# Kernel tuning notes

Hardware: AMD Instinct MI355X
Metric: run time of the kernel (lower is better)

## Reference

```python
import jax, jax.numpy as jnp
import numpy as np

N, D, T = 4096, 256, 8
RHO = 16.0
DT = 1.0 / T


def setup_inputs() -> dict:
    key = jax.random.key(0)
    k1, k2, k3, k4 = jax.random.split(key, 4)
    X = jax.random.normal(k1, (N, D), dtype=jnp.float32)
    # learned deformation parameters (small init so the Euler flow stays stable)
    A = jax.random.normal(k2, (T, N, D), dtype=jnp.float32) * 0.01
    A_aff = jax.random.normal(k3, (T, D, D), dtype=jnp.float32) * 0.01
    b_aff = jax.random.normal(k4, (T, D), dtype=jnp.float32) * 0.01
    return {"X": X, "A": A, "A_aff": A_aff, "b_aff": b_aff}


def _flow(X, A, A_aff, b_aff):
    inv_two_rho2 = 1.0 / (2.0 * RHO * RHO)

    def step(Z, params_t):
        A_t, Aaff_t, baff_t = params_t
        # Gaussian self-kernel K[i,j] = exp(-||z_i - z_j||^2 / (2 rho^2))
        sq = jnp.sum(Z * Z, axis=1)                      # [n]
        dist = sq[:, None] + sq[None, :] - 2.0 * (Z @ Z.T)  # [n, n]
        K = jnp.exp(-dist * inv_two_rho2)
        # velocity: affine part + RKHS (kernel message aggregation) part
        v = Z @ Aaff_t.T + baff_t[None, :] + K @ A_t     # [n, d]
        return Z + DT * v, None

    Z_final, _ = jax.lax.scan(step, X, (A, A_aff, b_aff))
    return Z_final


def reference(X, A, A_aff, b_aff):
    return _flow(X, A, A_aff, b_aff)
```

## Files before the change

kernel.cpp:

```cpp
#include <hip/hip_runtime.h>


#define N_PTS 4096
#define DIM   256
#define DT_C  0.125f
#define C1    (1.0f/512.0f)

typedef __bf16 bf16x8 __attribute__((ext_vector_type(8)));
typedef float  f32x16 __attribute__((ext_vector_type(16)));
typedef float  f32x4v __attribute__((ext_vector_type(4)));
typedef unsigned int   u32x4 __attribute__((ext_vector_type(4)));
typedef unsigned short u16x8 __attribute__((ext_vector_type(8)));

__device__ __forceinline__ unsigned short f2bf(float f) {
  unsigned int u = __builtin_bit_cast(unsigned int, f);
  u += 0x7fffu + ((u >> 16) & 1u);
  return (unsigned short)(u >> 16);
}
__device__ __forceinline__ float bf2f(unsigned short s) {
  unsigned int u = ((unsigned int)s) << 16;
  return __builtin_bit_cast(float, u);
}

__global__ __launch_bounds__(256) void k_prep(const float* __restrict__ A,
                                              unsigned short* __restrict__ ATf) {
  __shared__ float sT[64][36];
  const int jgrp = blockIdx.x, ds = blockIdx.y, t = blockIdx.z;
  const int tid = threadIdx.x;
  const float* Ab = A + (size_t)t * N_PTS * DIM;
  {
    const int j_l = tid >> 2, dq = tid & 3;
    const float* src = Ab + (size_t)(jgrp * 64 + j_l) * DIM + ds * 32 + dq * 8;
    f32x4v v0 = *(const f32x4v*)src, v1 = *(const f32x4v*)(src + 4);
    *(f32x4v*)&sT[j_l][dq * 8] = v0;
    *(f32x4v*)&sT[j_l][dq * 8 + 4] = v1;
  }
  __syncthreads();
  const int jb_l = tid >> 6, l = tid & 63, l31 = l & 31, lhi = l >> 5;
  u16x8 o;
#pragma unroll
  for (int e = 0; e < 8; ++e) o[e] = f2bf(sT[jb_l * 16 + lhi * 8 + e][l31]);
  unsigned short* dst = ATf + (size_t)t * (8 * 256 * 64 * 8)
                      + ((size_t)(ds * 256 + jgrp * 4 + jb_l) * 64 + l) * 8;
  *(u16x8*)dst = o;
}

__global__ __launch_bounds__(256) void k_init(const float* __restrict__ X,
                                              unsigned short* __restrict__ Zf,
                                              float* __restrict__ erow) {
  const int tid = threadIdx.x;
  const int r = blockIdx.x * 8 + (tid >> 5), o = tid & 31;
  const size_t base = (size_t)r * DIM + o * 8;
  f32x4v z0 = *(const f32x4v*)(X + base), z1 = *(const f32x4v*)(X + base + 4);
  u16x8 zb; float s = 0.f;
#pragma unroll
  for (int i = 0; i < 4; ++i) { zb[i] = f2bf(z0[i]); zb[4 + i] = f2bf(z1[i]);
                                s += z0[i] * z0[i] + z1[i] * z1[i]; }
  *(u16x8*)(Zf + ((size_t)((r >> 5) * 16 + (o >> 1)) * 64 + (o & 1) * 32 + (r & 31)) * 8) = zb;
#pragma unroll
  for (int d = 16; d > 0; d >>= 1) s += __shfl_down(s, d, 32);
  if (o == 0) erow[r] = __expf(-s * C1);
}

__global__ __launch_bounds__(512, 2) void k_flash(
    const unsigned short* __restrict__ Zf, const float* __restrict__ erow,
    const unsigned short* __restrict__ ATf_t,
    const float* __restrict__ Aaff_t,
    unsigned short* __restrict__ Opart) {
  __shared__ unsigned short sAj[3][32 * 512];
  __shared__ unsigned short sP[2][128 * 64];

  const int tid = threadIdx.x, lane = tid & 63, wid = tid >> 6;
  const int l31 = lane & 31, lhi = lane >> 5;
  const int chunk = blockIdx.x;
  const int i0 = blockIdx.y * 128;
  const int jb16 = chunk * 32;

#define STAGE(nt)                                                              \
  {                                                                            \
    unsigned short* dstb = sAj[(nt) % 3];                                      \
    _Pragma("unroll")                                                          \
    for (int q = 0; q < 4; ++q) {                                              \
      int s = wid * 4 + q;                                                     \
      int ds_ = s >> 2, ksl = s & 3;                                           \
      const unsigned short* src = ATf_t +                                      \
          ((size_t)(ds_ * 256 + jb16 + (nt) * 4 + ksl) * 64 + lane) * 8;       \
      *(u32x4*)&dstb[s * 512 + lane * 8] = *(const u32x4*)src;                 \
    }                                                                          \
  }

  STAGE(0);
  __syncthreads();

  if (wid < 4) {
    const int g1 = wid;
    bf16x8 af[16];
    {
      const unsigned short* ap = Zf + (((size_t)((i0 >> 5) + g1) * 16) * 64 + lane) * 8;
#pragma unroll
      for (int ks = 0; ks < 16; ++ks)
        af[ks] = __builtin_bit_cast(bf16x8, *(const u32x4*)(ap + ks * 512));
    }
    float eI[16];
#pragma unroll
    for (int c = 0; c < 16; ++c)
      eI[c] = erow[i0 + g1 * 32 + 4 * lhi + (c & 3) + 8 * (c >> 2)];

    for (int n = 0; n <= 8; ++n) {
      if (n < 8) {
        if (n < 7) STAGE(n + 1);
        f32x16 S0, S1;
#pragma unroll
        for (int i = 0; i < 16; ++i) { S0[i] = 0.f; S1[i] = 0.f; }
        {
          const unsigned short* bp =
              Zf + (((size_t)(chunk * 16 + n * 2) * 16) * 64 + lane) * 8;
#pragma unroll
          for (int ks = 0; ks < 16; ++ks) {
            bf16x8 b0 = __builtin_bit_cast(bf16x8, *(const u32x4*)(bp + ks * 512));
            bf16x8 b1 = __builtin_bit_cast(bf16x8, *(const u32x4*)(bp + 8192 + ks * 512));
            S0 = __builtin_amdgcn_mfma_f32_32x32x16_bf16(af[ks], b0, S0, 0, 0, 0);
            S1 = __builtin_amdgcn_mfma_f32_32x32x16_bf16(af[ks], b1, S1, 0, 0, 0);
          }
        }
        const int jj0 = chunk * 512 + n * 64;
        const float ej0 = erow[jj0 + l31];
        const float ej1 = erow[jj0 + 32 + l31];
        unsigned short* pb = sP[n & 1];
        const int blk0 = l31 >> 3, cl = l31 & 7;
#pragma unroll
        for (int c = 0; c < 16; ++c) {
          const int row = g1 * 32 + 4 * lhi + (c & 3) + 8 * (c >> 2);
          pb[row * 64 + ((blk0 ^ (row & 7)) * 8) + cl] =
              f2bf(eI[c] * ej0 * __expf(2.f * C1 * S0[c]));
          pb[row * 64 + (((4 + blk0) ^ (row & 7)) * 8) + cl] =
              f2bf(eI[c] * ej1 * __expf(2.f * C1 * S1[c]));
        }
      }
      __syncthreads();
    }
  } else {
    const int w4 = wid - 4;
    f32x16 Oa[4][2];
#pragma unroll
    for (int rs = 0; rs < 4; ++rs)
#pragma unroll
      for (int ct = 0; ct < 2; ++ct)
#pragma unroll
        for (int i = 0; i < 16; ++i) Oa[rs][ct][i] = 0.f;

    for (int n = 0; n <= 8; ++n) {
      if (n < 7) STAGE(n + 1);
      if (n == 0) {
#pragma unroll
        for (int q = 0; q < 2; ++q) {
          const int ksg = chunk * 2 + q;
          bf16x8 a[4];
#pragma unroll
          for (int rs = 0; rs < 4; ++rs)
            a[rs] = __builtin_bit_cast(bf16x8, *(const u32x4*)(
                Zf + (((size_t)((i0 >> 5) + rs) * 16 + ksg) * 64 + lane) * 8));
#pragma unroll
          for (int ct = 0; ct < 2; ++ct) {
            const int d = w4 * 64 + ct * 32 + l31;
            const float* bp = Aaff_t + (size_t)d * DIM + ksg * 16 + lhi * 8;
            f32x4v f0 = *(const f32x4v*)bp, f1 = *(const f32x4v*)(bp + 4);
            u16x8 tb;
#pragma unroll
            for (int i = 0; i < 4; ++i) { tb[i] = f2bf(f0[i]); tb[4 + i] = f2bf(f1[i]); }
            bf16x8 bv = __builtin_bit_cast(bf16x8, tb);
#pragma unroll
            for (int rs = 0; rs < 4; ++rs)
              Oa[rs][ct] = __builtin_amdgcn_mfma_f32_32x32x16_bf16(a[rs], bv, Oa[rs][ct], 0, 0, 0);
          }
        }
      }
      if (n >= 1) {
        const int m = n - 1;
        const unsigned short* aj = sAj[m % 3];
        const unsigned short* pb = sP[m & 1];
#pragma unroll
        for (int ks = 0; ks < 4; ++ks) {
          bf16x8 a[4], b[2];
          const int blk = ks * 2 + lhi;
#pragma unroll
          for (int rs = 0; rs < 4; ++rs) {
            const int row = rs * 32 + l31;
            a[rs] = *(const bf16x8*)&pb[row * 64 + ((blk ^ (row & 7)) * 8)];
          }
#pragma unroll
          for (int ct = 0; ct < 2; ++ct)
            b[ct] = *(const bf16x8*)&aj[((w4 * 2 + ct) * 4 + ks) * 512 + lane * 8];
#pragma unroll
          for (int rs = 0; rs < 4; ++rs)
#pragma unroll
            for (int ct = 0; ct < 2; ++ct)
              Oa[rs][ct] = __builtin_amdgcn_mfma_f32_32x32x16_bf16(a[rs], b[ct], Oa[rs][ct], 0, 0, 0);
        }
      }
      __syncthreads();
    }
    unsigned short* ob = Opart + (size_t)chunk * N_PTS * DIM + (size_t)w4 * 64 + l31;
#pragma unroll
    for (int rs = 0; rs < 4; ++rs)
#pragma unroll
      for (int cg = 0; cg < 4; ++cg) {
        const int rbase = rs * 32 + 4 * lhi + 8 * cg;
#pragma unroll
        for (int e = 0; e < 4; ++e) {
          const int c = cg * 4 + e;
          const size_t ro = (size_t)(i0 + rbase + e) * DIM;
          ob[ro]      = f2bf(Oa[rs][0][c]);
          ob[ro + 32] = f2bf(Oa[rs][1][c]);
        }
      }
  }
#undef STAGE
}

__global__ __launch_bounds__(256) void k_update(const float* __restrict__ Zin,
                                                const unsigned short* __restrict__ Opart,
                                                const float* __restrict__ baff_t,
                                                float* __restrict__ Zout,
                                                unsigned short* __restrict__ Zf,
                                                float* __restrict__ erow) {
  const int tid = threadIdx.x;
  const int r = blockIdx.x * 8 + (tid >> 5), o = tid & 31;
  const size_t base = (size_t)r * DIM + o * 8;
  f32x4v z0 = *(const f32x4v*)(Zin + base), z1 = *(const f32x4v*)(Zin + base + 4);
  f32x4v s0 = *(const f32x4v*)(baff_t + o * 8), s1 = *(const f32x4v*)(baff_t + o * 8 + 4);
#pragma unroll
  for (int c = 0; c < 8; ++c) {
    u16x8 p = *(const u16x8*)(Opart + (size_t)c * N_PTS * DIM + base);
#pragma unroll
    for (int i = 0; i < 4; ++i) { s0[i] += bf2f(p[i]); s1[i] += bf2f(p[4 + i]); }
  }
  u16x8 zb; float sv = 0.f;
#pragma unroll
  for (int i = 0; i < 4; ++i) {
    z0[i] += DT_C * s0[i]; z1[i] += DT_C * s1[i];
    zb[i] = f2bf(z0[i]); zb[4 + i] = f2bf(z1[i]);
    sv += z0[i] * z0[i] + z1[i] * z1[i];
  }
  *(f32x4v*)(Zout + base) = z0;
  *(f32x4v*)(Zout + base + 4) = z1;
  *(u16x8*)(Zf + ((size_t)((r >> 5) * 16 + (o >> 1)) * 64 + (o & 1) * 32 + (r & 31)) * 8) = zb;
#pragma unroll
  for (int d = 16; d > 0; d >>= 1) sv += __shfl_down(sv, d, 32);
  if (o == 0) erow[r] = __expf(-sv * C1);
}

extern "C" void kernel_launch(void* const* d_in, const int* in_sizes, int n_in,
                              void* d_out, int out_size, void* d_ws, size_t ws_size,
                              hipStream_t stream) {
  const float* X    = (const float*)d_in[0];
  const float* A    = (const float*)d_in[1];
  const float* Aaff = (const float*)d_in[2];
  const float* baff = (const float*)d_in[3];
  float* out = (float*)d_out;

  char* w = (char*)d_ws;
  size_t off = 0;
  unsigned short* ATf = (unsigned short*)(w + off); off += (size_t)8 * 8 * 256 * 64 * 8 * 2;
  unsigned short* Zf  = (unsigned short*)(w + off); off += (size_t)N_PTS * DIM * 2;
  float* erow = (float*)(w + off); off += (size_t)N_PTS * 4;
  float* Zf32 = (float*)(w + off); off += (size_t)N_PTS * DIM * 4;
  unsigned short* Opart = (unsigned short*)(w + off); off += (size_t)8 * N_PTS * DIM * 2;
  (void)ws_size; (void)in_sizes; (void)n_in; (void)out_size;

  k_prep<<<dim3(64, 8, 8), 256, 0, stream>>>(A, ATf);
  k_init<<<512, 256, 0, stream>>>(X, Zf, erow);

  const float* zin = X;
  for (int t = 0; t < 8; ++t) {
    float* zout = (t == 7) ? out : Zf32;
    k_flash<<<dim3(8, 32), 512, 0, stream>>>(
        Zf, erow, ATf + (size_t)t * (8 * 256 * 64 * 8), Aaff + (size_t)t * DIM * DIM, Opart);
    k_update<<<512, 256, 0, stream>>>(zin, Opart, baff + (size_t)t * DIM, zout, Zf, erow);
    zin = zout;
  }
}
```

Measured before the change: 430.3 us.

## Halve row tile per block, drop LDS staging of A, double grid

The flash kernel now handles 64 query rows per block instead of 128, and the launch grid doubles to 8x64 blocks. Each S-producing wave now computes one 32x32 tile instead of two. The triple-buffered shared-memory staging of the A operand is removed; consumer waves read A fragments directly from global memory. Launch bounds are raised to 4 blocks per CU. This is meant to improve occupancy and parallelism, but A is now re-read from global or L2 twice as often, and each block does less work per sync.

```diff
diff --git a/kernel.cpp b/kernel.cpp
--- a/kernel.cpp
+++ b/kernel.cpp
@@ -62,41 +62,24 @@
   if (o == 0) erow[r] = __expf(-s * C1);
 }
 
-__global__ __launch_bounds__(512, 2) void k_flash(
+__global__ __launch_bounds__(512, 4) void k_flash(
     const unsigned short* __restrict__ Zf, const float* __restrict__ erow,
     const unsigned short* __restrict__ ATf_t,
     const float* __restrict__ Aaff_t,
     unsigned short* __restrict__ Opart) {
-  __shared__ unsigned short sAj[3][32 * 512];
-  __shared__ unsigned short sP[2][128 * 64];
+  __shared__ unsigned short sP[2][64 * 64];
 
   const int tid = threadIdx.x, lane = tid & 63, wid = tid >> 6;
   const int l31 = lane & 31, lhi = lane >> 5;
   const int chunk = blockIdx.x;
-  const int i0 = blockIdx.y * 128;
-  const int jb16 = chunk * 32;
-
-#define STAGE(nt)                                                              \
-  {                                                                            \
-    unsigned short* dstb = sAj[(nt) % 3];                                      \
-    _Pragma("unroll")                                                          \
-    for (int q = 0; q < 4; ++q) {                                              \
-      int s = wid * 4 + q;                                                     \
-      int ds_ = s >> 2, ksl = s & 3;                                           \
-      const unsigned short* src = ATf_t +                                      \
-          ((size_t)(ds_ * 256 + jb16 + (nt) * 4 + ksl) * 64 + lane) * 8;       \
-      *(u32x4*)&dstb[s * 512 + lane * 8] = *(const u32x4*)src;                 \
-    }                                                                          \
-  }
-
-  STAGE(0);
-  __syncthreads();
+  const int i0 = blockIdx.y * 64;
+  const int ib = i0 >> 5;
 
   if (wid < 4) {
-    const int g1 = wid;
+    const int ip = wid >> 1, jh = wid & 1;
     bf16x8 af[16];
     {
-      const unsigned short* ap = Zf + (((size_t)((i0 >> 5) + g1) * 16) * 64 + lane) * 8;
+      const unsigned short* ap = Zf + ((size_t)(ib + ip) * 16 * 64 + lane) * 8;
 #pragma unroll
       for (int ks = 0; ks < 16; ++ks)
         af[ks] = __builtin_bit_cast(bf16x8, *(const u32x4*)(ap + ks * 512));
@@ -104,118 +87,102 @@
     float eI[16];
 #pragma unroll
     for (int c = 0; c < 16; ++c)
-      eI[c] = erow[i0 + g1 * 32 + 4 * lhi + (c & 3) + 8 * (c >> 2)];
-
-    for (int n = 0; n <= 8; ++n) {
-      if (n < 8) {
-        if (n < 7) STAGE(n + 1);
-        f32x16 S0, S1;
-#pragma unroll
-        for (int i = 0; i < 16; ++i) { S0[i] = 0.f; S1[i] = 0.f; }
-        {
-          const unsigned short* bp =
-              Zf + (((size_t)(chunk * 16 + n * 2) * 16) * 64 + lane) * 8;
-#pragma unroll
-          for (int ks = 0; ks < 16; ++ks) {
-            bf16x8 b0 = __builtin_bit_cast(bf16x8, *(const u32x4*)(bp + ks * 512));
-            bf16x8 b1 = __builtin_bit_cast(bf16x8, *(const u32x4*)(bp + 8192 + ks * 512));
-            S0 = __builtin_amdgcn_mfma_f32_32x32x16_bf16(af[ks], b0, S0, 0, 0, 0);
-            S1 = __builtin_amdgcn_mfma_f32_32x32x16_bf16(af[ks], b1, S1, 0, 0, 0);
-          }
+      eI[c] = erow[i0 + ip * 32 + 4 * lhi + (c & 3) + 8 * (c >> 2)];
+
+    for (int n = 0; n < 8; ++n) {
+      f32x16 S;
+#pragma unroll
+      for (int i = 0; i < 16; ++i) S[i] = 0.f;
+      {
+        const int jblk = chunk * 16 + n * 2 + jh;
+        const unsigned short* bp = Zf + ((size_t)jblk * 16 * 64 + lane) * 8;
+#pragma unroll
+        for (int ks = 0; ks < 16; ++ks) {
+          bf16x8 b = __builtin_bit_cast(bf16x8, *(const u32x4*)(bp + ks * 512));
+          S = __builtin_amdgcn_mfma_f32_32x32x16_bf16(af[ks], b, S, 0, 0, 0);
         }
-        const int jj0 = chunk * 512 + n * 64;
-        const float ej0 = erow[jj0 + l31];
-        const float ej1 = erow[jj0 + 32 + l31];
-        unsigned short* pb = sP[n & 1];
-        const int blk0 = l31 >> 3, cl = l31 & 7;
-#pragma unroll
-        for (int c = 0; c < 16; ++c) {
-          const int row = g1 * 32 + 4 * lhi + (c & 3) + 8 * (c >> 2);
-          pb[row * 64 + ((blk0 ^ (row & 7)) * 8) + cl] =
-              f2bf(eI[c] * ej0 * __expf(2.f * C1 * S0[c]));
-          pb[row * 64 + (((4 + blk0) ^ (row & 7)) * 8) + cl] =
-              f2bf(eI[c] * ej1 * __expf(2.f * C1 * S1[c]));
+      }
+      const float ej = erow[chunk * 512 + n * 64 + jh * 32 + l31];
+      unsigned short* pb = sP[n & 1];
+      const int blk = jh * 4 + (l31 >> 3), cl = l31 & 7;
+#pragma unroll
+      for (int c = 0; c < 16; ++c) {
+        const int row = ip * 32 + 4 * lhi + (c & 3) + 8 * (c >> 2);
+        pb[row * 64 + ((blk ^ (row & 7)) * 8) + cl] =
+            f2bf(eI[c] * ej * __expf(2.f * C1 * S[c]));
+      }
+      __syncthreads();
+    }
+    __syncthreads();
+  } else {
+    const int cd = wid - 4;
+    f32x16 O[2][2];
+#pragma unroll
+    for (int rs = 0; rs < 2; ++rs)
+#pragma unroll
+      for (int ct = 0; ct < 2; ++ct)
+#pragma unroll
+        for (int i = 0; i < 16; ++i) O[rs][ct][i] = 0.f;
+
+#pragma unroll
+    for (int q = 0; q < 2; ++q) {
+      const int ksg = chunk * 2 + q;
+      bf16x8 a[2];
+#pragma unroll
+      for (int rs = 0; rs < 2; ++rs)
+        a[rs] = __builtin_bit_cast(bf16x8, *(const u32x4*)(
+            Zf + (((size_t)(ib + rs) * 16 + ksg) * 64 + lane) * 8));
+#pragma unroll
+      for (int ct = 0; ct < 2; ++ct) {
+        const int d = cd * 64 + ct * 32 + l31;
+        const float* bp = Aaff_t + (size_t)d * DIM + ksg * 16 + lhi * 8;
+        f32x4v f0 = *(const f32x4v*)bp, f1 = *(const f32x4v*)(bp + 4);
+        u16x8 tb;
+#pragma unroll
+        for (int i = 0; i < 4; ++i) { tb[i] = f2bf(f0[i]); tb[4 + i] = f2bf(f1[i]); }
+        bf16x8 bv = __builtin_bit_cast(bf16x8, tb);
+#pragma unroll
+        for (int rs = 0; rs < 2; ++rs)
+          O[rs][ct] = __builtin_amdgcn_mfma_f32_32x32x16_bf16(a[rs], bv, O[rs][ct], 0, 0, 0);
+      }
+    }
+    __syncthreads();
+
+    for (int n = 1; n <= 8; ++n) {
+      const int m = n - 1;
+      const unsigned short* pb = sP[m & 1];
+#pragma unroll
+      for (int ks = 0; ks < 4; ++ks) {
+        bf16x8 a[2], b[2];
+        const int blk = ks * 2 + lhi;
+#pragma unroll
+        for (int rs = 0; rs < 2; ++rs) {
+          const int row = rs * 32 + l31;
+          a[rs] = *(const bf16x8*)&pb[row * 64 + ((blk ^ (row & 7)) * 8)];
         }
+#pragma unroll
+        for (int ct = 0; ct < 2; ++ct)
+          b[ct] = __builtin_bit_cast(bf16x8, *(const u32x4*)(ATf_t +
+              ((size_t)((cd * 2 + ct) * 256 + chunk * 32 + m * 4 + ks) * 64 + lane) * 8));
+#pragma unroll
+        for (int rs = 0; rs < 2; ++rs)
+#pragma unroll
+          for (int ct = 0; ct < 2; ++ct)
+            O[rs][ct] = __builtin_amdgcn_mfma_f32_32x32x16_bf16(a[rs], b[ct], O[rs][ct], 0, 0, 0);
       }
       __syncthreads();
     }
-  } else {
-    const int w4 = wid - 4;
-    f32x16 Oa[4][2];
-#pragma unroll
-    for (int rs = 0; rs < 4; ++rs)
-#pragma unroll
-      for (int ct = 0; ct < 2; ++ct)
-#pragma unroll
-        for (int i = 0; i < 16; ++i) Oa[rs][ct][i] = 0.f;
-
-    for (int n = 0; n <= 8; ++n) {
-      if (n < 7) STAGE(n + 1);
-      if (n == 0) {
-#pragma unroll
-        for (int q = 0; q < 2; ++q) {
-          const int ksg = chunk * 2 + q;
-          bf16x8 a[4];
-#pragma unroll
-          for (int rs = 0; rs < 4; ++rs)
-            a[rs] = __builtin_bit_cast(bf16x8, *(const u32x4*)(
-                Zf + (((size_t)((i0 >> 5) + rs) * 16 + ksg) * 64 + lane) * 8));
-#pragma unroll
-          for (int ct = 0; ct < 2; ++ct) {
-            const int d = w4 * 64 + ct * 32 + l31;
-            const float* bp = Aaff_t + (size_t)d * DIM + ksg * 16 + lhi * 8;
-            f32x4v f0 = *(const f32x4v*)bp, f1 = *(const f32x4v*)(bp + 4);
-            u16x8 tb;
-#pragma unroll
-            for (int i = 0; i < 4; ++i) { tb[i] = f2bf(f0[i]); tb[4 + i] = f2bf(f1[i]); }
-            bf16x8 bv = __builtin_bit_cast(bf16x8, tb);
-#pragma unroll
-            for (int rs = 0; rs < 4; ++rs)
-              Oa[rs][ct] = __builtin_amdgcn_mfma_f32_32x32x16_bf16(a[rs], bv, Oa[rs][ct], 0, 0, 0);
-          }
-        }
-      }
-      if (n >= 1) {
-        const int m = n - 1;
-        const unsigned short* aj = sAj[m % 3];
-        const unsigned short* pb = sP[m & 1];
-#pragma unroll
-        for (int ks = 0; ks < 4; ++ks) {
-          bf16x8 a[4], b[2];
-          const int blk = ks * 2 + lhi;
-#pragma unroll
-          for (int rs = 0; rs < 4; ++rs) {
-            const int row = rs * 32 + l31;
-            a[rs] = *(const bf16x8*)&pb[row * 64 + ((blk ^ (row & 7)) * 8)];
-          }
-#pragma unroll
-          for (int ct = 0; ct < 2; ++ct)
-            b[ct] = *(const bf16x8*)&aj[((w4 * 2 + ct) * 4 + ks) * 512 + lane * 8];
-#pragma unroll
-          for (int rs = 0; rs < 4; ++rs)
-#pragma unroll
-            for (int ct = 0; ct < 2; ++ct)
-              Oa[rs][ct] = __builtin_amdgcn_mfma_f32_32x32x16_bf16(a[rs], b[ct], Oa[rs][ct], 0, 0, 0);
-        }
-      }
-      __syncthreads();
-    }
-    unsigned short* ob = Opart + (size_t)chunk * N_PTS * DIM + (size_t)w4 * 64 + l31;
-#pragma unroll
-    for (int rs = 0; rs < 4; ++rs)
-#pragma unroll
-      for (int cg = 0; cg < 4; ++cg) {
-        const int rbase = rs * 32 + 4 * lhi + 8 * cg;
-#pragma unroll
-        for (int e = 0; e < 4; ++e) {
-          const int c = cg * 4 + e;
-          const size_t ro = (size_t)(i0 + rbase + e) * DIM;
-          ob[ro]      = f2bf(Oa[rs][0][c]);
-          ob[ro + 32] = f2bf(Oa[rs][1][c]);
-        }
-      }
-  }
-#undef STAGE
+
+    unsigned short* ob = Opart + (size_t)chunk * N_PTS * DIM + (size_t)cd * 64 + l31;
+#pragma unroll
+    for (int rs = 0; rs < 2; ++rs)
+#pragma unroll
+      for (int c = 0; c < 16; ++c) {
+        const int row = i0 + rs * 32 + 4 * lhi + (c & 3) + 8 * (c >> 2);
+        ob[(size_t)row * DIM]      = f2bf(O[rs][0][c]);
+        ob[(size_t)row * DIM + 32] = f2bf(O[rs][1][c]);
+      }
+  }
 }
 
 __global__ __launch_bounds__(256) void k_update(const float* __restrict__ Zin,
@@ -274,7 +241,7 @@
   const float* zin = X;
   for (int t = 0; t < 8; ++t) {
     float* zout = (t == 7) ? out : Zf32;
-    k_flash<<<dim3(8, 32), 512, 0, stream>>>(
+    k_flash<<<dim3(8, 64), 512, 0, stream>>>(
         Zf, erow, ATf + (size_t)t * (8 * 256 * 64 * 8), Aaff + (size_t)t * DIM * DIM, Opart);
     k_update<<<512, 256, 0, stream>>>(zin, Opart, baff + (size_t)t * DIM, zout, Zf, erow);
     zin = zout;
```

Measured after the change: 391.3 us. 1.1x faster.
